# Performance work log

Measured on AMD Instinct MI355X. Metric: run time of the kernel, lower is better.

Reference implementation:

```python
import jax, jax.numpy as jnp
import numpy as np

CL = 128   # context_length
IL = 64    # inst_length
PC = 256; CH1 = 256; CH2 = 256; CH3 = 256
CK1 = 3; CK2 = 3; CK3 = 3
F1 = 512; OUT = 1
F1_INPUT = CH3 * (CL - 1 - CK1 - CK2 - CK3 + 3)  # 256*121 = 30976
B = 2048


def _conv1d(x, w, b):
    # x: [B, Cin, L], w: [Cout, Cin, K] -> [B, Cout, L-K+1]
    y = jax.lax.conv_general_dilated(x, w, window_strides=(1,), padding='VALID',
                                     dimension_numbers=('NCH', 'OIH', 'NCH'))
    return y + b[None, :, None]


def setup_inputs() -> dict:
    key = jax.random.key(0)
    ks = jax.random.split(key, 13)
    def w(k, shape, fan_in):
        bound = 1.0 / np.sqrt(fan_in)
        return jax.random.uniform(k, shape, jnp.float32, -bound, bound)
    return {
        'x':   jax.random.normal(ks[0], (B, CL * IL), jnp.float32),
        'Wp':  w(ks[1], (PC, IL, 2), IL * 2),
        'bp':  w(ks[2], (PC,), IL * 2),
        'W1':  w(ks[3], (CH1, PC, CK1), PC * CK1),
        'b1':  w(ks[4], (CH1,), PC * CK1),
        'W2':  w(ks[5], (CH2, CH1, CK2), CH1 * CK2),
        'b2':  w(ks[6], (CH2,), CH1 * CK2),
        'W3':  w(ks[7], (CH3, CH2, CK3), CH2 * CK3),
        'b3':  w(ks[8], (CH3,), CH2 * CK3),
        'Wf1': w(ks[9], (F1, F1_INPUT), F1_INPUT),
        'bf1': w(ks[10], (F1,), F1_INPUT),
        'Wf2': w(ks[11], (OUT, F1), F1),
        'bf2': w(ks[12], (OUT,), F1),
    }


def reference(x, Wp, bp, W1, b1, W2, b2, W3, b3, Wf1, bf1, Wf2, bf2):
    # [B, CL*IL] -> [B, IL, CL]
    xt = x.reshape(-1, CL, IL).transpose(0, 2, 1)
    # Fused pairwise convp: the torch loop computes, for i in 1..CL-1,
    #   y[:, c, i-1] = sum_j Wp[c,j,0]*x[:,j,0] + Wp[c,j,1]*x[:,j,i] + bp[c]
    x0 = xt[:, :, 0]          # [B, IL]
    xr = xt[:, :, 1:]         # [B, IL, CL-1]
    y = (jnp.einsum('bj,cj->bc', x0, Wp[:, :, 0])[:, :, None]
         + jnp.einsum('bjl,cj->bcl', xr, Wp[:, :, 1])
         + bp[None, :, None])                       # [B, PC, CL-1]
    h = jax.nn.relu(y)
    h = jax.nn.relu(_conv1d(h, W1, b1))
    h = jax.nn.relu(_conv1d(h, W2, b2))
    h = jax.nn.relu(_conv1d(h, W3, b3))
    h = h.reshape(-1, F1_INPUT)
    h = jax.nn.relu(h @ Wf1.T + bf1)
    return h @ Wf2.T + bf2    # [B, OUT]
```

## Files before the change

### kernel.cpp

```cpp
#include <hip/hip_runtime.h>

typedef _Float16 f16;
typedef _Float16 f16x8 __attribute__((ext_vector_type(8)));
typedef _Float16 f16x4 __attribute__((ext_vector_type(4)));
typedef float    f32x4 __attribute__((ext_vector_type(4)));

#define B_SZ   2048
#define NCH    256
#define L0_    127
#define L1_    125
#define L2_    123
#define L3_    121
#define F1_    512
#define FCK    30976
#define KCH    968
#define SPLIT  22
#define KPS    44
#define NS_FC  22
#define BUFF   16384

__device__ __forceinline__ void gl16(const f16* g, f16* l) {
    __builtin_amdgcn_global_load_lds(
        (const __attribute__((address_space(1))) void*)g,
        (__attribute__((address_space(3))) void*)l, 16, 0, 0);
}

__global__ __launch_bounds__(256) void prep_w(const float* __restrict__ Wp,
                                              const float* __restrict__ W1,
                                              const float* __restrict__ W2,
                                              const float* __restrict__ W3,
                                              f16* __restrict__ wpw,
                                              f16* __restrict__ wct1,
                                              f16* __restrict__ wct2,
                                              f16* __restrict__ wct3) {
    int g = blockIdx.x;
    if (g < 128) {
        int idx = g * 256 + threadIdx.x;
        int ck = idx >> 13, co = (idx >> 5) & 255, w5 = idx & 31;
        int j = ck * 32 + w5;
        float v = (j < 64) ? Wp[co * 128 + j * 2 + 1]
                           : Wp[co * 128 + (j - 64) * 2];
        wpw[idx] = (f16)v;
        return;
    }
    int g2 = g - 128;
    const float* W = (g2 < 768) ? W1 : (g2 < 1536) ? W2 : W3;
    f16* dst = (g2 < 768) ? wct1 : (g2 < 1536) ? wct2 : wct3;
    int idx = (g2 % 768) * 256 + threadIdx.x;
    int ck = idx >> 13, co = (idx >> 5) & 255, w5 = idx & 31;
    int kt = ck * 32 + w5;
    int k = kt >> 8, ci = kt & 255;
    dst[idx] = (f16)W[((size_t)co * NCH + ci) * 3 + k];
}

__global__ __launch_bounds__(256) void prep_wf1k(const float* __restrict__ Wf1,
                                                 f16* __restrict__ wf1h) {
    __shared__ f16 t[NCH * 122];
    const int f = blockIdx.x, tid = threadIdx.x;
    const float* src = Wf1 + (size_t)f * FCK;
    for (int idx = tid; idx < FCK; idx += 256) {
        int co = idx / 121, l = idx - co * 121;
        t[co * 122 + l] = (f16)src[idx];
    }
    __syncthreads();
    f16* dst = wf1h + (size_t)f * FCK;
    for (int idx = tid; idx < FCK; idx += 256) {
        int l = idx >> 8, co = idx & 255;
        dst[idx] = t[co * 122 + l];
    }
}

#define STAGEB(WT, S2, BUF)                                                   \
  {                                                                           \
    const f16* src0_ = (WT) + (size_t)(2 * (S2)) * 8192;                      \
    _Pragma("unroll")                                                         \
    for (int j = 0; j < 8; ++j) {                                             \
        int u_ = j * 256 + w * 64 + lane;                                     \
        int row_ = u_ >> 2, cu_ = u_ & 3;                                     \
        int cs_ = cu_ ^ ((row_ >> 2) & 3);                                    \
        gl16(src0_ + row_ * 32 + cs_ * 8,                                     \
             wlds + (BUF) * BUFF + (size_t)(j * 256 + w * 64) * 8);           \
    }                                                                         \
  }

#define GEMM_LAYER(WT, NS, CSTEPS)                                            \
  _Pragma("unroll")                                                           \
  for (int m = 0; m < 8; ++m)                                                 \
    _Pragma("unroll")                                                         \
    for (int n = 0; n < 4; ++n) acc[m][n] = (f32x4){0.f, 0.f, 0.f, 0.f};      \
  _Pragma("unroll 1")                                                         \
  for (int s = 0; s < (NS); ++s) {                                            \
    const int cur = s & 1;                                                    \
    if (s + 1 < (NS)) STAGEB(WT, s + 1, cur ^ 1)                              \
    __builtin_amdgcn_sched_barrier(0);                                        \
    _Pragma("unroll")                                                         \
    for (int kk = 0; kk < 2; ++kk) {                                          \
      const int ks32 = 2 * s + kk;                                            \
      const int k = ks32 / (CSTEPS), cb = (ks32 % (CSTEPS)) * 4;              \
      f16x8 a[8], bf[4];                                                      \
      _Pragma("unroll")                                                       \
      for (int m = 0; m < 8; ++m) {                                           \
        const int r_ = 16 * m + lr + k;                                       \
        a[m] = *(const f16x8*)(ins + r_ * 256 + (((cb + lh) ^ (r_ & 7)) << 3)); \
      }                                                                       \
      _Pragma("unroll")                                                       \
      for (int n = 0; n < 4; ++n) {                                           \
        const int co = wc0 + 16 * n + lr;                                     \
        bf[n] = *(const f16x8*)(wlds + cur * BUFF + kk * 8192                 \
                                + (co * 4 + (lh ^ ((co >> 2) & 3))) * 8);     \
      }                                                                       \
      __builtin_amdgcn_s_setprio(1);                                          \
      _Pragma("unroll")                                                       \
      for (int n = 0; n < 4; ++n)                                             \
        _Pragma("unroll")                                                     \
        for (int m = 0; m < 8; ++m)                                           \
          acc[m][n] = __builtin_amdgcn_mfma_f32_16x16x32_f16(a[m], bf[n],     \
                                                             acc[m][n], 0, 0, 0); \
      __builtin_amdgcn_s_setprio(0);                                          \
    }                                                                         \
    __builtin_amdgcn_sched_barrier(0);                                        \
    asm volatile("s_waitcnt vmcnt(0)" ::: "memory");                          \
    __builtin_amdgcn_sched_barrier(0);                                        \
    __builtin_amdgcn_s_barrier();                                             \
  }

#define EPI_LDS(BIAS, LOUT)                                                   \
  {                                                                           \
    _Pragma("unroll")                                                         \
    for (int n = 0; n < 4; ++n) {                                             \
      const int co = wc0 + 16 * n + lr;                                       \
      const float e = (BIAS)[co];                                             \
      const int sl = co >> 3, el = co & 7;                                    \
      _Pragma("unroll")                                                       \
      for (int m = 0; m < 8; ++m)                                             \
        _Pragma("unroll")                                                     \
        for (int r = 0; r < 4; ++r) {                                         \
          const int l = 16 * m + lh * 4 + r;                                  \
          if (l < (LOUT)) {                                                   \
            float v = fmaxf(acc[m][n][r] + e, 0.f);                           \
            ins[l * 256 + (((sl) ^ (l & 7)) << 3) + el] = (f16)v;             \
          }                                                                   \
        }                                                                     \
    }                                                                         \
  }

__global__ __launch_bounds__(256, 1) void fused_conv(
        const float* __restrict__ xin,
        const f16* __restrict__ wpw,  const float* __restrict__ bp,
        const f16* __restrict__ wct1, const float* __restrict__ b1,
        const f16* __restrict__ wct2, const float* __restrict__ b2,
        const f16* __restrict__ wct3, const float* __restrict__ b3,
        f16* __restrict__ h3out) {
    __shared__ f16 ins[130 * 256];
    __shared__ f16 wlds[2 * BUFF];

    const int b    = blockIdx.x;
    const int tid  = threadIdx.x;
    const int lane = tid & 63, w = tid >> 6;
    const int wc0  = w * 64;
    const int lr   = lane & 15, lh = lane >> 4;

    f32x4 acc[8][4];

    STAGEB(wpw, 0, 0)
    {
        const float* xr = xin + (size_t)b * 8192;
        for (int u = tid; u < 130 * 16; u += 256) {
            int r = u >> 4, sl = u & 15;
            int off = (sl < 8)
                ? ((r + 1 < 128 ? (r + 1) * 64 : 127 * 64) + sl * 8)
                : (sl - 8) * 8;
            float4 v0 = *(const float4*)(xr + off);
            float4 v1 = *(const float4*)(xr + off + 4);
            f16x8 h = { (f16)v0.x, (f16)v0.y, (f16)v0.z, (f16)v0.w,
                        (f16)v1.x, (f16)v1.y, (f16)v1.z, (f16)v1.w };
            *(f16x8*)(ins + r * 256 + ((sl ^ (r & 7)) << 3)) = h;
        }
    }
    __syncthreads();

    GEMM_LAYER(wpw, 2, 4)
    STAGEB(wct1, 0, 0)
    EPI_LDS(bp, L0_)
    asm volatile("s_waitcnt vmcnt(0) lgkmcnt(0)" ::: "memory");
    __builtin_amdgcn_s_barrier();

    GEMM_LAYER(wct1, 12, 8)
    STAGEB(wct2, 0, 0)
    EPI_LDS(b1, L1_)
    asm volatile("s_waitcnt vmcnt(0) lgkmcnt(0)" ::: "memory");
    __builtin_amdgcn_s_barrier();

    GEMM_LAYER(wct2, 12, 8)
    STAGEB(wct3, 0, 0)
    EPI_LDS(b2, L2_)
    asm volatile("s_waitcnt vmcnt(0) lgkmcnt(0)" ::: "memory");
    __builtin_amdgcn_s_barrier();

    GEMM_LAYER(wct3, 12, 8)
    {
        f16* ob = h3out + (size_t)b * L3_ * NCH;
#pragma unroll
        for (int n = 0; n < 4; ++n) {
            const int co = wc0 + 16 * n + lr;
            const float e = b3[co];
#pragma unroll
            for (int m = 0; m < 8; ++m)
#pragma unroll
                for (int r = 0; r < 4; ++r) {
                    const int l = 16 * m + lh * 4 + r;
                    if (l < L3_) {
                        float v = fmaxf(acc[m][n][r] + e, 0.f);
                        ob[(size_t)l * NCH + co] = (f16)v;
                    }
                }
        }
    }
}

__global__ __launch_bounds__(512, 1) void fc1k(const f16* __restrict__ A,
                                               const f16* __restrict__ Bw,
                                               float* __restrict__ part,
                                               int CB) {
    __shared__ f16 Asl[2 * 8192];
    __shared__ f16 Bsl[2 * 16384];
    const int m0 = blockIdx.x * 128, n0 = blockIdx.y * 256, sp = blockIdx.z;
    const int tid  = threadIdx.x;
    const int lane = tid & 63, w = tid >> 6;
    const int wb0  = (w >> 2) * 64, wf0 = (w & 3) * 64;
    const int lr   = lane & 15, lh = lane >> 4;
    const int ck0  = sp * KPS;

    auto stage = [&](int s2, int buf) {
        const int k0 = (ck0 + 2 * s2) * 32;
#pragma unroll
        for (int j = 0; j < 2; ++j) {
            int u = j * 512 + tid;
            int row = u >> 3, cu = u & 7;
            int cs = cu ^ (row & 7);
            gl16(A + (size_t)(m0 + row) * FCK + k0 + cs * 8,
                 Asl + buf * 8192 + (size_t)(j * 512 + w * 64) * 8);
        }
#pragma unroll
        for (int j = 0; j < 4; ++j) {
            int u = j * 512 + tid;
            int row = u >> 3, cu = u & 7;
            int cs = cu ^ (row & 7);
            gl16(Bw + (size_t)(n0 + row) * FCK + k0 + cs * 8,
                 Bsl + buf * 16384 + (size_t)(j * 512 + w * 64) * 8);
        }
    };

    f32x4 acc[4][4];
#pragma unroll
    for (int m = 0; m < 4; ++m)
#pragma unroll
        for (int n = 0; n < 4; ++n) acc[m][n] = (f32x4){0.f, 0.f, 0.f, 0.f};

    stage(0, 0);
    __syncthreads();

#pragma unroll 1
    for (int s = 0; s < NS_FC; ++s) {
        const int cur = s & 1;
        if (s + 1 < NS_FC) stage(s + 1, cur ^ 1);
        __builtin_amdgcn_sched_barrier(0);
#pragma unroll
        for (int kk = 0; kk < 2; ++kk) {
            f16x8 a[4], bf[4];
#pragma unroll
            for (int m = 0; m < 4; ++m) {
                const int row = wb0 + 16 * m + lr;
                const int un = (kk * 4 + lh) ^ (row & 7);
                a[m] = *(const f16x8*)(Asl + cur * 8192 + row * 64 + un * 8);
            }
#pragma unroll
            for (int n = 0; n < 4; ++n) {
                const int row = wf0 + 16 * n + lr;
                const int un = (kk * 4 + lh) ^ (row & 7);
                bf[n] = *(const f16x8*)(Bsl + cur * 16384 + row * 64 + un * 8);
            }
            __builtin_amdgcn_s_setprio(1);
#pragma unroll
            for (int m = 0; m < 4; ++m)
#pragma unroll
                for (int n = 0; n < 4; ++n)
                    acc[m][n] = __builtin_amdgcn_mfma_f32_16x16x32_f16(
                        a[m], bf[n], acc[m][n], 0, 0, 0);
            __builtin_amdgcn_s_setprio(0);
        }
        __builtin_amdgcn_sched_barrier(0);
        asm volatile("s_waitcnt vmcnt(0)" ::: "memory");
        __builtin_amdgcn_sched_barrier(0);
        __builtin_amdgcn_s_barrier();
    }

#pragma unroll
    for (int m = 0; m < 4; ++m)
#pragma unroll
        for (int n = 0; n < 4; ++n)
#pragma unroll
            for (int r = 0; r < 4; ++r) {
                const int bl = m0 + wb0 + 16 * m + lh * 4 + r;
                const int f  = n0 + wf0 + 16 * n + lr;
                part[((size_t)sp * CB + bl) * F1_ + f] = acc[m][n][r];
            }
}

__global__ __launch_bounds__(512) void fcout(const float* __restrict__ part,
                                             const float* __restrict__ bf1,
                                             const float* __restrict__ Wf2,
                                             const float* __restrict__ bf2,
                                             float* __restrict__ out,
                                             int CB) {
    __shared__ float red[8];
    const int m = blockIdx.x;
    const int f = threadIdx.x;
    float s = bf1[f];
#pragma unroll
    for (int sp = 0; sp < SPLIT; ++sp)
        s += part[((size_t)sp * CB + m) * F1_ + f];
    float p = fmaxf(s, 0.f) * Wf2[f];
#pragma unroll
    for (int o = 32; o > 0; o >>= 1) p += __shfl_xor(p, o);
    if ((f & 63) == 0) red[f >> 6] = p;
    __syncthreads();
    if (f < 8) {
        float v = red[f];
        v += __shfl_xor(v, 1);
        v += __shfl_xor(v, 2);
        v += __shfl_xor(v, 4);
        if (f == 0) out[m] = v + bf2[0];
    }
}

extern "C" void kernel_launch(void* const* d_in, const int* in_sizes, int n_in,
                              void* d_out, int out_size, void* d_ws, size_t ws_size,
                              hipStream_t stream) {
    const float* x   = (const float*)d_in[0];
    const float* Wp  = (const float*)d_in[1];
    const float* bp  = (const float*)d_in[2];
    const float* W1  = (const float*)d_in[3];
    const float* b1  = (const float*)d_in[4];
    const float* W2  = (const float*)d_in[5];
    const float* b2  = (const float*)d_in[6];
    const float* W3  = (const float*)d_in[7];
    const float* b3  = (const float*)d_in[8];
    const float* Wf1 = (const float*)d_in[9];
    const float* bf1 = (const float*)d_in[10];
    const float* Wf2 = (const float*)d_in[11];
    const float* bf2 = (const float*)d_in[12];
    float* out = (float*)d_out;

    char* base = (char*)d_ws;
    size_t off = 0;
    auto alloc = [&](size_t bytes) {
        size_t o = off; off = (off + bytes + 255) & ~(size_t)255; return o;
    };
    const size_t o_wpw  = alloc((size_t)NCH * 128 * 2);
    const size_t o_wct1 = alloc((size_t)NCH * 768 * 2);
    const size_t o_wct2 = alloc((size_t)NCH * 768 * 2);
    const size_t o_wct3 = alloc((size_t)NCH * 768 * 2);
    const size_t o_wf1h = alloc((size_t)F1_ * FCK * 2);
    const size_t fixed  = off;

    int CB = 0;
    const int cand[5] = {2048, 1024, 512, 256, 128};
    for (int i = 0; i < 5; ++i) {
        size_t c = (size_t)cand[i];
        size_t need = fixed
            + (((size_t)SPLIT * c * F1_ * 4 + 255) & ~(size_t)255)
            + ((c * (size_t)L3_ * NCH * 2 + 255) & ~(size_t)255);
        if (need <= ws_size) { CB = cand[i]; break; }
    }
    if (CB == 0) return;
    const int nchunk = B_SZ / CB;

    const size_t o_part = alloc((size_t)SPLIT * CB * F1_ * 4);
    const size_t o_h3   = alloc((size_t)CB * L3_ * NCH * 2);

    f16*   wpw  = (f16*)(base + o_wpw);
    f16*   wct1 = (f16*)(base + o_wct1);
    f16*   wct2 = (f16*)(base + o_wct2);
    f16*   wct3 = (f16*)(base + o_wct3);
    f16*   wf1h = (f16*)(base + o_wf1h);
    float* part = (float*)(base + o_part);
    f16*   h3   = (f16*)(base + o_h3);

    prep_w<<<2432, 256, 0, stream>>>(Wp, W1, W2, W3, wpw, wct1, wct2, wct3);
    prep_wf1k<<<F1_, 256, 0, stream>>>(Wf1, wf1h);

    for (int c = 0; c < nchunk; ++c) {
        const size_t b0 = (size_t)c * CB;
        fused_conv<<<CB, 256, 0, stream>>>(x + b0 * 8192,
                                           wpw, bp, wct1, b1, wct2, b2,
                                           wct3, b3, h3);
        fc1k<<<dim3(CB / 128, 2, SPLIT), 512, 0, stream>>>(h3, wf1h, part, CB);
        fcout<<<CB, 512, 0, stream>>>(part, bf1, Wf2, bf2, out + b0, CB);
    }
}
```

Baseline: 649.4 us.

## Triple-buffer conv weight staging and double-buffer register fragments across k-steps

Replaces the double-buffered two-k-step-per-barrier weight staging with a three-slot ring of single k-step weight tiles. Each step issues the load two steps ahead, waits with a partial vmcnt, and prefetches the next A/B fragments from LDS into registers while the current MFMAs run. The goal is to hide global-to-LDS latency and LDS read latency behind matrix work. The cost is one barrier per k-step instead of per two steps, and twice the fragment registers, which raises register pressure.

After: 665.4 us. 2.5% more time.

```diff
diff --git a/kernel.cpp b/kernel.cpp
--- a/kernel.cpp
+++ b/kernel.cpp
@@ -17,7 +17,6 @@
 #define SPLIT  22
 #define KPS    44
 #define NS_FC  22
-#define BUFF   16384
 
 __device__ __forceinline__ void gl16(const f16* g, f16* l) {
     __builtin_amdgcn_global_load_lds(
@@ -70,59 +69,73 @@
     }
 }
 
-#define STAGEB(WT, S2, BUF)                                                   \
-  {                                                                           \
-    const f16* src0_ = (WT) + (size_t)(2 * (S2)) * 8192;                      \
-    _Pragma("unroll")                                                         \
-    for (int j = 0; j < 8; ++j) {                                             \
-        int u_ = j * 256 + w * 64 + lane;                                     \
-        int row_ = u_ >> 2, cu_ = u_ & 3;                                     \
-        int cs_ = cu_ ^ ((row_ >> 2) & 3);                                    \
-        gl16(src0_ + row_ * 32 + cs_ * 8,                                     \
-             wlds + (BUF) * BUFF + (size_t)(j * 256 + w * 64) * 8);           \
-    }                                                                         \
-  }
-
-#define GEMM_LAYER(WT, NS, CSTEPS)                                            \
+#define STAGEC(WT, KS, BUF)                                                   \
+  { const f16* s0_ = (WT) + (size_t)(KS) * 8192;                              \
+    _Pragma("unroll")                                                         \
+    for (int j = 0; j < 4; ++j) {                                             \
+      int u_ = j * 256 + tid;                                                 \
+      int r_ = u_ >> 2, c_ = u_ & 3, cs_ = c_ ^ ((r_ >> 2) & 3);              \
+      gl16(s0_ + r_ * 32 + cs_ * 8,                                           \
+           wlds + (BUF) * 8192 + (size_t)(j * 256 + w * 64) * 8); } }
+
+#define READF(FA, FB, KS, CSTEPS)                                             \
+  { const int kn_ = (KS) / (CSTEPS), cb_ = ((KS) % (CSTEPS)) * 4;             \
+    const int rb_ = (KS) % 3;                                                 \
+    _Pragma("unroll")                                                         \
+    for (int m = 0; m < 8; ++m) {                                             \
+      const int r_ = 16 * m + lr + kn_;                                       \
+      FA[m] = *(const f16x8*)(ins + r_ * 256                                  \
+                              + (((cb_ + lh) ^ (r_ & 7)) << 3)); }            \
+    _Pragma("unroll")                                                         \
+    for (int n = 0; n < 4; ++n) {                                             \
+      const int co_ = wc0 + 16 * n + lr;                                      \
+      FB[n] = *(const f16x8*)(wlds + rb_ * 8192                               \
+                + (co_ * 4 + (lh ^ ((co_ >> 2) & 3))) * 8); } }
+
+#define MFMA32(FA, FB)                                                        \
+  __builtin_amdgcn_s_setprio(1);                                              \
+  _Pragma("unroll")                                                           \
+  for (int n = 0; n < 4; ++n)                                                 \
+    _Pragma("unroll")                                                         \
+    for (int m = 0; m < 8; ++m)                                               \
+      acc[m][n] = __builtin_amdgcn_mfma_f32_16x16x32_f16(FA[m], FB[n],        \
+                                                         acc[m][n], 0, 0, 0); \
+  __builtin_amdgcn_s_setprio(0);
+
+#define BODY(FCa, FCb, FNa, FNb, S, WT, CSTEPS)                               \
+  STAGEC(WT, (S) + 2, ((S) + 2) % 3)                                          \
+  __builtin_amdgcn_sched_barrier(0);                                          \
+  asm volatile("s_waitcnt vmcnt(4) lgkmcnt(0)" ::: "memory");                 \
+  __builtin_amdgcn_sched_barrier(0);                                          \
+  __builtin_amdgcn_s_barrier();                                               \
+  __builtin_amdgcn_sched_barrier(0);                                          \
+  READF(FNa, FNb, (S) + 1, CSTEPS)                                            \
+  __builtin_amdgcn_sched_barrier(0);                                          \
+  MFMA32(FCa, FCb)                                                            \
+  __builtin_amdgcn_sched_barrier(0);
+
+#define LAYER_LOOP(WT, NS, CSTEPS)                                            \
   _Pragma("unroll")                                                           \
   for (int m = 0; m < 8; ++m)                                                 \
     _Pragma("unroll")                                                         \
     for (int n = 0; n < 4; ++n) acc[m][n] = (f32x4){0.f, 0.f, 0.f, 0.f};      \
   _Pragma("unroll 1")                                                         \
-  for (int s = 0; s < (NS); ++s) {                                            \
-    const int cur = s & 1;                                                    \
-    if (s + 1 < (NS)) STAGEB(WT, s + 1, cur ^ 1)                              \
-    __builtin_amdgcn_sched_barrier(0);                                        \
-    _Pragma("unroll")                                                         \
-    for (int kk = 0; kk < 2; ++kk) {                                          \
-      const int ks32 = 2 * s + kk;                                            \
-      const int k = ks32 / (CSTEPS), cb = (ks32 % (CSTEPS)) * 4;              \
-      f16x8 a[8], bf[4];                                                      \
-      _Pragma("unroll")                                                       \
-      for (int m = 0; m < 8; ++m) {                                           \
-        const int r_ = 16 * m + lr + k;                                       \
-        a[m] = *(const f16x8*)(ins + r_ * 256 + (((cb + lh) ^ (r_ & 7)) << 3)); \
-      }                                                                       \
-      _Pragma("unroll")                                                       \
-      for (int n = 0; n < 4; ++n) {                                           \
-        const int co = wc0 + 16 * n + lr;                                     \
-        bf[n] = *(const f16x8*)(wlds + cur * BUFF + kk * 8192                 \
-                                + (co * 4 + (lh ^ ((co >> 2) & 3))) * 8);     \
-      }                                                                       \
-      __builtin_amdgcn_s_setprio(1);                                          \
-      _Pragma("unroll")                                                       \
-      for (int n = 0; n < 4; ++n)                                             \
-        _Pragma("unroll")                                                     \
-        for (int m = 0; m < 8; ++m)                                           \
-          acc[m][n] = __builtin_amdgcn_mfma_f32_16x16x32_f16(a[m], bf[n],     \
-                                                             acc[m][n], 0, 0, 0); \
-      __builtin_amdgcn_s_setprio(0);                                          \
-    }                                                                         \
-    __builtin_amdgcn_sched_barrier(0);                                        \
-    asm volatile("s_waitcnt vmcnt(0)" ::: "memory");                          \
-    __builtin_amdgcn_sched_barrier(0);                                        \
-    __builtin_amdgcn_s_barrier();                                             \
-  }
+  for (int s = 0; s < (NS) - 2; s += 2) {                                     \
+    BODY(aC, bC, aN, bN, s, WT, CSTEPS)                                       \
+    BODY(aN, bN, aC, bC, s + 1, WT, CSTEPS)                                   \
+  }                                                                           \
+                          \
+  asm volatile("s_waitcnt vmcnt(0) lgkmcnt(0)" ::: "memory");                 \
+  __builtin_amdgcn_sched_barrier(0);                                          \
+  __builtin_amdgcn_s_barrier();                                               \
+  __builtin_amdgcn_sched_barrier(0);                                          \
+  READF(aN, bN, (NS) - 1, CSTEPS)                                             \
+  __builtin_amdgcn_sched_barrier(0);                                          \
+  MFMA32(aC, bC)                                                              \
+  __builtin_amdgcn_sched_barrier(0);                                          \
+             \
+  MFMA32(aN, bN)                                                              \
+  __builtin_amdgcn_sched_barrier(0);
 
 #define EPI_LDS(BIAS, LOUT)                                                   \
   {                                                                           \
@@ -144,6 +157,20 @@
     }                                                                         \
   }
 
+#define BOUNDARY(BIAS, LOUT, NEXTWT)                                          \
+  STAGEC(NEXTWT, 0, 0)                                                        \
+  STAGEC(NEXTWT, 1, 1)                                                        \
+  __builtin_amdgcn_sched_barrier(0);                                          \
+  __builtin_amdgcn_s_barrier();                                               \
+  __builtin_amdgcn_sched_barrier(0);                                          \
+  EPI_LDS(BIAS, LOUT)                                                         \
+  __builtin_amdgcn_sched_barrier(0);                                          \
+  asm volatile("s_waitcnt vmcnt(0) lgkmcnt(0)" ::: "memory");                 \
+  __builtin_amdgcn_sched_barrier(0);                                          \
+  __builtin_amdgcn_s_barrier();                                               \
+  __builtin_amdgcn_sched_barrier(0);                                          \
+  READF(aC, bC, 0, 8)
+
 __global__ __launch_bounds__(256, 1) void fused_conv(
         const float* __restrict__ xin,
         const f16* __restrict__ wpw,  const float* __restrict__ bp,
@@ -152,7 +179,7 @@
         const f16* __restrict__ wct3, const float* __restrict__ b3,
         f16* __restrict__ h3out) {
     __shared__ f16 ins[130 * 256];
-    __shared__ f16 wlds[2 * BUFF];
+    __shared__ f16 wlds[3 * 8192];
 
     const int b    = blockIdx.x;
     const int tid  = threadIdx.x;
@@ -161,8 +188,10 @@
     const int lr   = lane & 15, lh = lane >> 4;
 
     f32x4 acc[8][4];
-
-    STAGEB(wpw, 0, 0)
+    f16x8 aC[8], bC[4], aN[8], bN[4];
+
+    STAGEC(wpw, 0, 0)
+    STAGEC(wpw, 1, 1)
     {
         const float* xr = xin + (size_t)b * 8192;
         for (int u = tid; u < 130 * 16; u += 256) {
@@ -178,26 +207,18 @@
         }
     }
     __syncthreads();
-
-    GEMM_LAYER(wpw, 2, 4)
-    STAGEB(wct1, 0, 0)
-    EPI_LDS(bp, L0_)
-    asm volatile("s_waitcnt vmcnt(0) lgkmcnt(0)" ::: "memory");
-    __builtin_amdgcn_s_barrier();
-
-    GEMM_LAYER(wct1, 12, 8)
-    STAGEB(wct2, 0, 0)
-    EPI_LDS(b1, L1_)
-    asm volatile("s_waitcnt vmcnt(0) lgkmcnt(0)" ::: "memory");
-    __builtin_amdgcn_s_barrier();
-
-    GEMM_LAYER(wct2, 12, 8)
-    STAGEB(wct3, 0, 0)
-    EPI_LDS(b2, L2_)
-    asm volatile("s_waitcnt vmcnt(0) lgkmcnt(0)" ::: "memory");
-    __builtin_amdgcn_s_barrier();
-
-    GEMM_LAYER(wct3, 12, 8)
+    READF(aC, bC, 0, 4)
+
+    LAYER_LOOP(wpw, 4, 4)
+    BOUNDARY(bp, L0_, wct1)
+
+    LAYER_LOOP(wct1, 24, 8)
+    BOUNDARY(b1, L1_, wct2)
+
+    LAYER_LOOP(wct2, 24, 8)
+    BOUNDARY(b2, L2_, wct3)
+
+    LAYER_LOOP(wct3, 24, 8)
     {
         f16* ob = h3out + (size_t)b * L3_ * NCH;
 #pragma unroll
```

## Pad FC1 K dimension and restage conv3 output through LDS with vector stores

Applied to the files above, without the earlier changes.

Pads the FC1 reduction length from 121 to 124 rows per sample (zero-filled in both the h3 activations and the reordered Wf1). This lets the split-K be 16 ways of 31 steps instead of 22 ways of 22 steps, which changes the grid size, the number of partial sums and the per-block work. The conv3 epilogue now goes through the LDS epilogue and writes rows as 16-byte vectors instead of scattered 2-byte stores. The padding adds a little extra FC1 work and memory in exchange for fewer partials and coalesced writes.

Measured after the change: 631.1 us. 2.8% less time.

```diff
diff --git a/kernel.cpp b/kernel.cpp
--- a/kernel.cpp
+++ b/kernel.cpp
@@ -13,10 +13,10 @@
 #define L3_    121
 #define F1_    512
 #define FCK    30976
-#define KCH    968
-#define SPLIT  22
-#define KPS    44
-#define NS_FC  22
+#define FCK2   31744
+#define SPLIT  16
+#define KPS2   62
+#define NS_FC  31
 #define BUFF   16384
 
 __device__ __forceinline__ void gl16(const f16* g, f16* l) {
@@ -63,10 +63,10 @@
         t[co * 122 + l] = (f16)src[idx];
     }
     __syncthreads();
-    f16* dst = wf1h + (size_t)f * FCK;
-    for (int idx = tid; idx < FCK; idx += 256) {
+    f16* dst = wf1h + (size_t)f * FCK2;
+    for (int idx = tid; idx < FCK2; idx += 256) {
         int l = idx >> 8, co = idx & 255;
-        dst[idx] = t[co * 122 + l];
+        dst[idx] = (l < 121) ? t[co * 122 + l] : (f16)0.f;
     }
 }
 
@@ -198,22 +198,19 @@
     __builtin_amdgcn_s_barrier();
 
     GEMM_LAYER(wct3, 12, 8)
+    EPI_LDS(b3, L3_)
+    asm volatile("s_waitcnt lgkmcnt(0)" ::: "memory");
+    __builtin_amdgcn_s_barrier();
     {
-        f16* ob = h3out + (size_t)b * L3_ * NCH;
-#pragma unroll
-        for (int n = 0; n < 4; ++n) {
-            const int co = wc0 + 16 * n + lr;
-            const float e = b3[co];
-#pragma unroll
-            for (int m = 0; m < 8; ++m)
-#pragma unroll
-                for (int r = 0; r < 4; ++r) {
-                    const int l = 16 * m + lh * 4 + r;
-                    if (l < L3_) {
-                        float v = fmaxf(acc[m][n][r] + e, 0.f);
-                        ob[(size_t)l * NCH + co] = (f16)v;
-                    }
-                }
+        f16* ob = h3out + (size_t)b * FCK2;
+        const f16x8 z = { (f16)0.f, (f16)0.f, (f16)0.f, (f16)0.f,
+                          (f16)0.f, (f16)0.f, (f16)0.f, (f16)0.f };
+        for (int u = tid; u < 124 * 32; u += 256) {
+            int r = u >> 5, sl = u & 31;
+            f16x8 v = (r < L3_)
+                ? *(const f16x8*)(ins + r * 256 + ((sl ^ (r & 7)) << 3))
+                : z;
+            *(f16x8*)(ob + r * 256 + sl * 8) = v;
         }
     }
 }
@@ -229,7 +226,7 @@
     const int lane = tid & 63, w = tid >> 6;
     const int wb0  = (w >> 2) * 64, wf0 = (w & 3) * 64;
     const int lr   = lane & 15, lh = lane >> 4;
-    const int ck0  = sp * KPS;
+    const int ck0  = sp * KPS2;
 
     auto stage = [&](int s2, int buf) {
         const int k0 = (ck0 + 2 * s2) * 32;
@@ -238,7 +235,7 @@
             int u = j * 512 + tid;
             int row = u >> 3, cu = u & 7;
             int cs = cu ^ (row & 7);
-            gl16(A + (size_t)(m0 + row) * FCK + k0 + cs * 8,
+            gl16(A + (size_t)(m0 + row) * FCK2 + k0 + cs * 8,
                  Asl + buf * 8192 + (size_t)(j * 512 + w * 64) * 8);
         }
 #pragma unroll
@@ -246,7 +243,7 @@
             int u = j * 512 + tid;
             int row = u >> 3, cu = u & 7;
             int cs = cu ^ (row & 7);
-            gl16(Bw + (size_t)(n0 + row) * FCK + k0 + cs * 8,
+            gl16(Bw + (size_t)(n0 + row) * FCK2 + k0 + cs * 8,
                  Bsl + buf * 16384 + (size_t)(j * 512 + w * 64) * 8);
         }
     };
@@ -361,7 +358,7 @@
     const size_t o_wct1 = alloc((size_t)NCH * 768 * 2);
     const size_t o_wct2 = alloc((size_t)NCH * 768 * 2);
     const size_t o_wct3 = alloc((size_t)NCH * 768 * 2);
-    const size_t o_wf1h = alloc((size_t)F1_ * FCK * 2);
+    const size_t o_wf1h = alloc((size_t)F1_ * FCK2 * 2);
     const size_t fixed  = off;
 
     int CB = 0;
@@ -370,14 +367,14 @@
         size_t c = (size_t)cand[i];
         size_t need = fixed
             + (((size_t)SPLIT * c * F1_ * 4 + 255) & ~(size_t)255)
-            + ((c * (size_t)L3_ * NCH * 2 + 255) & ~(size_t)255);
+            + ((c * (size_t)FCK2 * 2 + 255) & ~(size_t)255);
         if (need <= ws_size) { CB = cand[i]; break; }
     }
     if (CB == 0) return;
     const int nchunk = B_SZ / CB;
 
     const size_t o_part = alloc((size_t)SPLIT * CB * F1_ * 4);
-    const size_t o_h3   = alloc((size_t)CB * L3_ * NCH * 2);
+    const size_t o_h3   = alloc((size_t)CB * FCK2 * 2);
 
     f16*   wpw  = (f16*)(base + o_wpw);
     f16*   wct1 = (f16*)(base + o_wct1);
```
